# Kernel tuning notes

Measured on AMD Instinct MI355X. Metric: run time of the kernel, lower is better.

The kernel has to match this reference:

```python
import jax, jax.numpy as jnp
import numpy as np

N_NODES = 100000
N_EDGES = 1600000
IN_CH = 128
EDGE_CH = 16
OUT_CH = 64
H1, F1 = 8, 8          # gat1: heads=8, out=8, concat -> 64
NEG_SLOPE = 0.2


def _add_self_loops(edge_index, n):
    sl = jnp.arange(n, dtype=edge_index.dtype)
    return jnp.concatenate([edge_index, jnp.stack([sl, sl])], axis=1)


def gat_layer(x, edge_index, W, a_src, a_dst, b, heads, out_dim, concat):
    """PyG-style GATConv (eval mode, self-loops already included in edge_index)."""
    n = x.shape[0]
    src, dst = edge_index[0], edge_index[1]
    xW = (x @ W).reshape(n, heads, out_dim)          # [N,H,F]
    al_src = (xW * a_src).sum(-1)                    # [N,H]
    al_dst = (xW * a_dst).sum(-1)                    # [N,H]
    e = jax.nn.leaky_relu(al_src[src] + al_dst[dst], NEG_SLOPE)  # [E,H]
    # segment softmax over incoming edges of each dst node
    m = jnp.full((n, heads), -jnp.inf, e.dtype).at[dst].max(e)
    w = jnp.exp(e - m[dst])
    denom = jax.ops.segment_sum(w, dst, num_segments=n)
    alpha = w / (denom[dst] + 1e-16)                 # [E,H]
    out = jax.ops.segment_sum(xW[src] * alpha[..., None], dst, num_segments=n)
    out = out.reshape(n, heads * out_dim) if concat else out.mean(axis=1)
    return out + b


def setup_inputs() -> dict:
    key = jax.random.key(0)
    ks = jax.random.split(key, 16)
    p = lambda k, shp: (jax.random.normal(k, shp, jnp.float32) * 0.1)
    inp = {
        "x": jax.random.normal(ks[0], (N_NODES, IN_CH), jnp.float32),
        "edge_index": jax.random.randint(ks[1], (2, N_EDGES), 0, N_NODES, jnp.int64 if jax.config.jax_enable_x64 else jnp.int32),
        "edge_attr": jax.random.normal(ks[2], (N_EDGES, EDGE_CH), jnp.float32),
        "W1": p(ks[3], (IN_CH, H1 * F1)),
        "a_src1": p(ks[4], (H1, F1)),
        "a_dst1": p(ks[5], (H1, F1)),
        "b1": jnp.zeros((H1 * F1,), jnp.float32),
        "W2": p(ks[6], (H1 * F1, OUT_CH)),
        "a_src2": p(ks[7], (1, OUT_CH)),
        "a_dst2": p(ks[8], (1, OUT_CH)),
        "b2": jnp.zeros((OUT_CH,), jnp.float32),
        "lin_W": p(ks[9], (OUT_CH, OUT_CH)),
        "lin_b": jnp.zeros((OUT_CH,), jnp.float32),
        "mlp_W1": p(ks[10], (2 * OUT_CH + EDGE_CH, 128)),
        "mlp_b1": jnp.zeros((128,), jnp.float32),
        "mlp_W2": p(ks[11], (128, 2)),
        "mlp_b2": jnp.zeros((2,), jnp.float32),
    }
    return inp


def reference(x, edge_index, edge_attr, W1, a_src1, a_dst1, b1, W2, a_src2, a_dst2, b2,
              lin_W, lin_b, mlp_W1, mlp_b1, mlp_W2, mlp_b2):
    n = x.shape[0]
    ei_sl = _add_self_loops(edge_index, n)
    h = gat_layer(x, ei_sl, W1, a_src1, a_dst1, b1, H1, F1, concat=True)
    h = jax.nn.elu(h)
    h = gat_layer(h, ei_sl, W2, a_src2, a_dst2, b2, 1, OUT_CH, concat=False)
    h = jax.nn.elu(h)
    h = h @ lin_W + lin_b                              # [N, out]
    src, dst = edge_index[0], edge_index[1]
    ef = jnp.concatenate([h[src], h[dst], edge_attr], axis=1)  # [E, 2*out+edge_ch]
    eo = jax.nn.relu(ef @ mlp_W1 + mlp_b1) @ mlp_W2 + mlp_b2   # [E, 2]
    return jax.nn.log_softmax(eo, axis=1)
```

## Files before the change

kernel.cpp:

```cpp
#include <hip/hip_runtime.h>
#include <math.h>

#define DEV_INLINE __device__ __forceinline__
typedef unsigned short ushort;
typedef __attribute__((ext_vector_type(8))) short bf16x8;
typedef __attribute__((ext_vector_type(4))) float f32x4;

DEV_INLINE float lrelu(float x){ return x > 0.f ? x : 0.2f*x; }
DEV_INLINE float eluf(float x){ return x>0.f? x : (__expf(x)-1.f); }
DEV_INLINE ushort f2bf(float f){
  unsigned u = __float_as_uint(f);
  return (ushort)((u + 0x7FFFu + ((u>>16)&1u)) >> 16);
}

__global__ __launch_bounds__(256) void gemm_n64(const float* __restrict__ A, const float* __restrict__ W,
    const float* __restrict__ bias, float* __restrict__ C, ushort* __restrict__ Cb, int n, int K)
{
  int j = threadIdx.x & 63;
  int node = blockIdx.x*4 + (threadIdx.x>>6);
  if (node >= n) return;
  const float4* A4 = (const float4*)(A + (size_t)node*K);
  float acc = 0.f;
  int K4 = K>>2;
  for (int k4 = 0; k4 < K4; ++k4) {
    float4 a = A4[k4];
    const float* w = W + k4*256 + j;
    acc = fmaf(a.x, w[0],   acc);
    acc = fmaf(a.y, w[64],  acc);
    acc = fmaf(a.z, w[128], acc);
    acc = fmaf(a.w, w[192], acc);
  }
  if (bias) acc += bias[j];
  if (C)  C[(size_t)node*64 + j] = acc;
  if (Cb) Cb[(size_t)node*64 + j] = f2bf(acc);
}

__global__ __launch_bounds__(256) void hist_kernel(const int* __restrict__ dst, int* __restrict__ deg, int E)
{
  int e = blockIdx.x*blockDim.x + threadIdx.x;
  if (e < E) atomicAdd(deg + dst[e], 1);
}

__global__ __launch_bounds__(256) void scan_p1(const int* __restrict__ deg, int* __restrict__ part, int n)
{
  __shared__ int red[256];
  int base = blockIdx.x*1024;
  int s = 0;
  for (int k = threadIdx.x; k < 1024; k += 256) { int i = base+k; s += (i<n)? deg[i] : 0; }
  red[threadIdx.x] = s; __syncthreads();
  for (int off = 128; off > 0; off >>= 1) {
    if (threadIdx.x < off) red[threadIdx.x] += red[threadIdx.x+off];
    __syncthreads();
  }
  if (threadIdx.x == 0) part[blockIdx.x] = red[0];
}

__global__ void scan_p2(int* part, int* rowptr, int nb, int n)
{
  if (threadIdx.x == 0 && blockIdx.x == 0) {
    int run = 0;
    for (int b = 0; b < nb; ++b) { int v = part[b]; part[b] = run; run += v; }
    rowptr[n] = run;
  }
}

__global__ __launch_bounds__(256) void scan_p3(const int* __restrict__ deg, const int* __restrict__ part,
    int* __restrict__ rowptr, int n)
{
  __shared__ int ts[256];
  int tid = threadIdx.x;
  int base = blockIdx.x*1024 + tid*4;
  int v0=0,v1=0,v2=0,v3=0;
  if (base+0 < n) v0 = deg[base+0];
  if (base+1 < n) v1 = deg[base+1];
  if (base+2 < n) v2 = deg[base+2];
  if (base+3 < n) v3 = deg[base+3];
  ts[tid] = v0+v1+v2+v3; __syncthreads();
  for (int off = 1; off < 256; off <<= 1) {
    int t = (tid >= off) ? ts[tid-off] : 0;
    __syncthreads();
    ts[tid] += t;
    __syncthreads();
  }
  int ex = part[blockIdx.x] + (tid ? ts[tid-1] : 0);
  if (base+0 < n) { rowptr[base+0] = ex; ex += v0; }
  if (base+1 < n) { rowptr[base+1] = ex; ex += v1; }
  if (base+2 < n) { rowptr[base+2] = ex; ex += v2; }
  if (base+3 < n) { rowptr[base+3] = ex; ex += v3; }
}

__global__ __launch_bounds__(256) void copy_int(const int* __restrict__ a, int* __restrict__ b, int n)
{
  int i = blockIdx.x*blockDim.x + threadIdx.x;
  if (i < n) b[i] = a[i];
}

__global__ __launch_bounds__(256) void scatter_kernel(const int* __restrict__ src, const int* __restrict__ dst,
    int* __restrict__ cursor, int* __restrict__ csr, int E)
{
  int e = blockIdx.x*blockDim.x + threadIdx.x;
  if (e >= E) return;
  int pos = atomicAdd(cursor + dst[e], 1);
  csr[pos] = src[e];
}

__global__ __launch_bounds__(256) void al_init1(const float* __restrict__ xW, const float* __restrict__ a_src,
    const float* __restrict__ a_dst, float* __restrict__ alS, float* __restrict__ alD, int n)
{
  int t = blockIdx.x*blockDim.x + threadIdx.x;
  if (t >= n*8) return;
  int h = t & 7;
  const float4* xw4 = (const float4*)(xW + (size_t)(t>>3)*64 + h*8);
  float4 x0 = xw4[0], x1 = xw4[1];
  const float4* as4 = (const float4*)(a_src + h*8);
  const float4* ad4 = (const float4*)(a_dst + h*8);
  float4 s0 = as4[0], s1 = as4[1], d0 = ad4[0], d1 = ad4[1];
  alS[t] = x0.x*s0.x + x0.y*s0.y + x0.z*s0.z + x0.w*s0.w
         + x1.x*s1.x + x1.y*s1.y + x1.z*s1.z + x1.w*s1.w;
  alD[t] = x0.x*d0.x + x0.y*d0.y + x0.z*d0.z + x0.w*d0.w
         + x1.x*d1.x + x1.y*d1.y + x1.z*d1.z + x1.w*d1.w;
}

__global__ __launch_bounds__(256) void al_init2(const float* __restrict__ xW, const float* __restrict__ a_src,
    const float* __restrict__ a_dst, float* __restrict__ alS, float* __restrict__ alD, int n)
{
  int node = blockIdx.x*blockDim.x + threadIdx.x;
  if (node >= n) return;
  const float4* xw4 = (const float4*)(xW + (size_t)node*64);
  const float4* as4 = (const float4*)a_src;
  const float4* ad4 = (const float4*)a_dst;
  float s = 0.f, d = 0.f;
  #pragma unroll
  for (int q = 0; q < 16; ++q) {
    float4 v = xw4[q], a = as4[q], bb = ad4[q];
    s += v.x*a.x + v.y*a.y + v.z*a.z + v.w*a.w;
    d += v.x*bb.x + v.y*bb.y + v.z*bb.z + v.w*bb.w;
  }
  alS[node] = s; alD[node] = d;
}

__global__ __launch_bounds__(256) void agg1(const float* __restrict__ xW, const float* __restrict__ alS,
    const float* __restrict__ alD, const int* __restrict__ rowptr, const int* __restrict__ csr,
    const float* __restrict__ b, float* __restrict__ outp, int n)
{
  int node = blockIdx.x*4 + (threadIdx.x>>6);
  if (node >= n) return;
  int l = threadIdx.x & 63, h = l >> 3;
  float aD  = alD[(size_t)node*8 + h];
  float m   = lrelu(alS[(size_t)node*8 + h] + aD);
  float den = 1.f;
  float acc = xW[(size_t)node*64 + l];
  int p0 = rowptr[node], p1 = rowptr[node+1];
  for (int p = p0; p < p1; ++p) {
    int s = csr[p];
    float e  = lrelu(alS[(size_t)s*8 + h] + aD);
    float xv = xW[(size_t)s*64 + l];
    float mn = fmaxf(m, e);
    float sc = __expf(m - mn);
    float w  = __expf(e - mn);
    den = den*sc + w;
    acc = acc*sc + w*xv;
    m = mn;
  }
  outp[(size_t)node*64 + l] = eluf(acc/(den + 1e-16f) + b[l]);
}

__global__ __launch_bounds__(256) void agg2(const float* __restrict__ xW, const float* __restrict__ alS,
    const float* __restrict__ alD, const int* __restrict__ rowptr, const int* __restrict__ csr,
    const float* __restrict__ b, float* __restrict__ outp, int n)
{
  int node = blockIdx.x*4 + (threadIdx.x>>6);
  if (node >= n) return;
  int l = threadIdx.x & 63;
  float aD  = alD[node];
  float m   = lrelu(alS[node] + aD);
  float den = 1.f;
  float acc = xW[(size_t)node*64 + l];
  int p0 = rowptr[node], p1 = rowptr[node+1];
  for (int p = p0; p < p1; ++p) {
    int s = csr[p];
    float e  = lrelu(alS[s] + aD);
    float xv = xW[(size_t)s*64 + l];
    float mn = fmaxf(m, e);
    float sc = __expf(m - mn);
    float w  = __expf(e - mn);
    den = den*sc + w;
    acc = acc*sc + w*xv;
    m = mn;
  }
  outp[(size_t)node*64 + l] = eluf(acc/(den + 1e-16f) + b[l]);
}

__global__ __launch_bounds__(256) void attr2bf(const float* __restrict__ attr, ushort* __restrict__ attrb, int n4)
{
  int t = blockIdx.x*blockDim.x + threadIdx.x;
  if (t >= n4) return;
  float4 a = ((const float4*)attr)[t];
  ushort4 o; o.x = f2bf(a.x); o.y = f2bf(a.y); o.z = f2bf(a.z); o.w = f2bf(a.w);
  ((ushort4*)attrb)[t] = o;
}

__global__ void w1_swizzle(const float* __restrict__ W1, ushort* __restrict__ w1sw)
{
  int t = blockIdx.x*blockDim.x + threadIdx.x;
  if (t >= 2560) return;
  int l = t & 63, nk = t >> 6;
  int nt = nk/5, ks = nk - nt*5;
  int ncol = nt*16 + (l&15);
  int kb = ks*32 + (l>>4)*8;
  union { ushort u[8]; uint4 q; } v;
  #pragma unroll
  for (int j = 0; j < 8; ++j) {
    int k = kb + j;
    float f = (k < 144) ? W1[k*128 + ncol] : 0.f;
    v.u[j] = f2bf(f);
  }
  ((uint4*)w1sw)[t] = v.q;
}

__global__ __launch_bounds__(256) void edge_mlp_mfma(
    const ushort* __restrict__ h3b, const ushort* __restrict__ attrb,
    const int* __restrict__ src, const int* __restrict__ dst,
    const ushort* __restrict__ w1sw, const float* __restrict__ b1,
    const float* __restrict__ W2, const float* __restrict__ b2,
    float* __restrict__ out, int E)
{
  __shared__ uint4 W1s[2560];
  for (int i = threadIdx.x; i < 2560; i += 256) W1s[i] = ((const uint4*)w1sw)[i];
  __syncthreads();
  const bf16x8* Bf = (const bf16x8*)W1s;

  const int lane = threadIdx.x & 63;
  const int quad = lane >> 4, l15 = lane & 15;

  float w2a[8], w2b[8], bia[8];
  #pragma unroll
  for (int nt = 0; nt < 8; ++nt) {
    w2a[nt] = W2[(nt*16 + l15)*2 + 0];
    w2b[nt] = W2[(nt*16 + l15)*2 + 1];
    bia[nt] = b1[nt*16 + l15];
  }
  const float bb0 = b2[0], bb1 = b2[1];

  const int wid = (blockIdx.x*256 + threadIdx.x) >> 6;
  const int nw  = gridDim.x*4;
  const int nT  = (E + 15) >> 4;

  for (int t = wid; t < nT; t += nw) {
    const int tb = t*16;
    int e = tb + l15; if (e >= E) e = E - 1;
    const int s = src[e], d = dst[e];

    bf16x8 a0 = *(const bf16x8*)(h3b + (size_t)s*64 + quad*8);
    bf16x8 a1 = *(const bf16x8*)(h3b + (size_t)s*64 + 32 + quad*8);
    bf16x8 a2 = *(const bf16x8*)(h3b + (size_t)d*64 + quad*8);
    bf16x8 a3 = *(const bf16x8*)(h3b + (size_t)d*64 + 32 + quad*8);
    bf16x8 a4 = {};
    if (quad < 2) a4 = *(const bf16x8*)(attrb + (size_t)e*16 + quad*8);

    f32x4 acc[8];
    #pragma unroll
    for (int nt = 0; nt < 8; ++nt) acc[nt] = (f32x4){0.f,0.f,0.f,0.f};

    #pragma unroll
    for (int nt = 0; nt < 8; ++nt) {
      acc[nt] = __builtin_amdgcn_mfma_f32_16x16x32_bf16(a0, Bf[(nt*5+0)*64 + lane], acc[nt], 0,0,0);
      acc[nt] = __builtin_amdgcn_mfma_f32_16x16x32_bf16(a1, Bf[(nt*5+1)*64 + lane], acc[nt], 0,0,0);
      acc[nt] = __builtin_amdgcn_mfma_f32_16x16x32_bf16(a2, Bf[(nt*5+2)*64 + lane], acc[nt], 0,0,0);
      acc[nt] = __builtin_amdgcn_mfma_f32_16x16x32_bf16(a3, Bf[(nt*5+3)*64 + lane], acc[nt], 0,0,0);
      acc[nt] = __builtin_amdgcn_mfma_f32_16x16x32_bf16(a4, Bf[(nt*5+4)*64 + lane], acc[nt], 0,0,0);
    }

    #pragma unroll
    for (int r = 0; r < 4; ++r) {
      float p0 = 0.f, p1 = 0.f;
      #pragma unroll
      for (int nt = 0; nt < 8; ++nt) {
        float hv = fmaxf(acc[nt][r] + bia[nt], 0.f);
        p0 = fmaf(hv, w2a[nt], p0);
        p1 = fmaf(hv, w2b[nt], p1);
      }
      #pragma unroll
      for (int off = 1; off < 16; off <<= 1) {
        p0 += __shfl_xor(p0, off, 64);
        p1 += __shfl_xor(p1, off, 64);
      }
      if (l15 == 0) {
        int eo = tb + quad*4 + r;
        if (eo < E) {
          p0 += bb0; p1 += bb1;
          float mm = fmaxf(p0, p1);
          float ls = mm + __logf(__expf(p0-mm) + __expf(p1-mm));
          ((float2*)out)[eo] = make_float2(p0 - ls, p1 - ls);
        }
      }
    }
  }
}

extern "C" void kernel_launch(void* const* d_in, const int* in_sizes, int n_in,
                              void* d_out, int out_size, void* d_ws, size_t ws_size,
                              hipStream_t stream) {
  const float* x      = (const float*)d_in[0];
  const int*   ei     = (const int*)d_in[1];
  const float* attr   = (const float*)d_in[2];
  const float* W1     = (const float*)d_in[3];
  const float* a_src1 = (const float*)d_in[4];
  const float* a_dst1 = (const float*)d_in[5];
  const float* b1     = (const float*)d_in[6];
  const float* W2     = (const float*)d_in[7];
  const float* a_src2 = (const float*)d_in[8];
  const float* a_dst2 = (const float*)d_in[9];
  const float* b2     = (const float*)d_in[10];
  const float* linW   = (const float*)d_in[11];
  const float* linb   = (const float*)d_in[12];
  const float* mW1    = (const float*)d_in[13];
  const float* mb1    = (const float*)d_in[14];
  const float* mW2    = (const float*)d_in[15];
  const float* mb2    = (const float*)d_in[16];
  float* out = (float*)d_out;

  int N = in_sizes[0] / 128;
  int E = in_sizes[1] / 2;
  const int* src = ei;
  const int* dst = ei + E;

  char* ws = (char*)d_ws;
  float*    bufA   = (float*)(ws);
  float*    bufH   = (float*)(ws + 25600000);
  int*      csr    = (int*)  (ws + 51200000);
  float*    alS1   = (float*)(ws + 57600000);
  float*    alD1   = (float*)(ws + 60800000);
  int*      rowptr = (int*)  (ws + 64000000);
  int*      degcur = (int*)  (ws + 64400064);
  int*      part   = (int*)  (ws + 64800064);
  ushort*   w1sw   = (ushort*)(ws + 64900096);
  float*    alS2   = (float*)(ws + 57600000);
  float*    alD2   = (float*)(ws + 58000000);
  ushort*   h3b    = (ushort*)(ws + 51200000);
  ushort*   attrb  = (ushort*)(ws);

  int gN4 = (N + 3) / 4;
  int gNH = (N*8 + 255) / 256;
  int gN  = (N + 255) / 256;
  int gE  = (E + 255) / 256;
  int nChunk = (N + 1023) / 1024;

  hipMemsetAsync(degcur, 0, (size_t)N*sizeof(int), stream);
  hist_kernel<<<gE, 256, 0, stream>>>(dst, degcur, E);
  scan_p1<<<nChunk, 256, 0, stream>>>(degcur, part, N);
  scan_p2<<<1, 64, 0, stream>>>(part, rowptr, nChunk, N);
  scan_p3<<<nChunk, 256, 0, stream>>>(degcur, part, rowptr, N);
  copy_int<<<gN, 256, 0, stream>>>(rowptr, degcur, N);
  scatter_kernel<<<gE, 256, 0, stream>>>(src, dst, degcur, csr, E);
  w1_swizzle<<<10, 256, 0, stream>>>(mW1, w1sw);

  gemm_n64<<<gN4, 256, 0, stream>>>(x, W1, nullptr, bufA, nullptr, N, 128);
  al_init1<<<gNH, 256, 0, stream>>>(bufA, a_src1, a_dst1, alS1, alD1, N);
  agg1<<<gN4, 256, 0, stream>>>(bufA, alS1, alD1, rowptr, csr, b1, bufH, N);
  gemm_n64<<<gN4, 256, 0, stream>>>(bufH, W2, nullptr, bufA, nullptr, N, 64);
  al_init2<<<gN, 256, 0, stream>>>(bufA, a_src2, a_dst2, alS2, alD2, N);
  agg2<<<gN4, 256, 0, stream>>>(bufA, alS2, alD2, rowptr, csr, b2, bufH, N);
  gemm_n64<<<gN4, 256, 0, stream>>>(bufH, linW, linb, nullptr, h3b, N, 64);
  attr2bf<<<(E*4 + 255)/256, 256, 0, stream>>>(attr, attrb, E*4);
  edge_mlp_mfma<<<1024, 256, 0, stream>>>(h3b, attrb, src, dst, w1sw, mb1, mW2, mb2, out, E);
}
```

Baseline: 1.336 ms.

## Store GAT features in bf16, fuse attr conversion and cursor copy, unroll aggregation

The node-feature buffers xW for both GAT layers are now stored as bf16, halving gather traffic in the aggregation kernels and the attention-logit kernels. The separate copy_int and attr2bf kernels are removed: the scan writes the cursor directly, and edge_attr is converted to bf16 inside the edge MLP. The aggregation loops are unrolled by two, and the edge MLP gets more blocks and an occupancy hint. The bf16 storage lowers the precision of intermediate features.

```diff
diff --git a/kernel.cpp b/kernel.cpp
--- a/kernel.cpp
+++ b/kernel.cpp
@@ -12,9 +12,10 @@
   unsigned u = __float_as_uint(f);
   return (ushort)((u + 0x7FFFu + ((u>>16)&1u)) >> 16);
 }
+DEV_INLINE float b2f(ushort u){ return __uint_as_float(((unsigned)u)<<16); }
 
 __global__ __launch_bounds__(256) void gemm_n64(const float* __restrict__ A, const float* __restrict__ W,
-    const float* __restrict__ bias, float* __restrict__ C, ushort* __restrict__ Cb, int n, int K)
+    const float* __restrict__ bias, ushort* __restrict__ Cb, int n, int K)
 {
   int j = threadIdx.x & 63;
   int node = blockIdx.x*4 + (threadIdx.x>>6);
@@ -31,8 +32,7 @@
     acc = fmaf(a.w, w[192], acc);
   }
   if (bias) acc += bias[j];
-  if (C)  C[(size_t)node*64 + j] = acc;
-  if (Cb) Cb[(size_t)node*64 + j] = f2bf(acc);
+  Cb[(size_t)node*64 + j] = f2bf(acc);
 }
 
 __global__ __launch_bounds__(256) void hist_kernel(const int* __restrict__ dst, int* __restrict__ deg, int E)
@@ -65,7 +65,7 @@
 }
 
 __global__ __launch_bounds__(256) void scan_p3(const int* __restrict__ deg, const int* __restrict__ part,
-    int* __restrict__ rowptr, int n)
+    int* __restrict__ rowptr, int* __restrict__ cursor, int n)
 {
   __shared__ int ts[256];
   int tid = threadIdx.x;
@@ -83,16 +83,10 @@
     __syncthreads();
   }
   int ex = part[blockIdx.x] + (tid ? ts[tid-1] : 0);
-  if (base+0 < n) { rowptr[base+0] = ex; ex += v0; }
-  if (base+1 < n) { rowptr[base+1] = ex; ex += v1; }
-  if (base+2 < n) { rowptr[base+2] = ex; ex += v2; }
-  if (base+3 < n) { rowptr[base+3] = ex; ex += v3; }
-}
-
-__global__ __launch_bounds__(256) void copy_int(const int* __restrict__ a, int* __restrict__ b, int n)
-{
-  int i = blockIdx.x*blockDim.x + threadIdx.x;
-  if (i < n) b[i] = a[i];
+  if (base+0 < n) { rowptr[base+0] = ex; cursor[base+0] = ex; ex += v0; }
+  if (base+1 < n) { rowptr[base+1] = ex; cursor[base+1] = ex; ex += v1; }
+  if (base+2 < n) { rowptr[base+2] = ex; cursor[base+2] = ex; ex += v2; }
+  if (base+3 < n) { rowptr[base+3] = ex; cursor[base+3] = ex; ex += v3; }
 }
 
 __global__ __launch_bounds__(256) void scatter_kernel(const int* __restrict__ src, const int* __restrict__ dst,
@@ -104,42 +98,44 @@
   csr[pos] = src[e];
 }
 
-__global__ __launch_bounds__(256) void al_init1(const float* __restrict__ xW, const float* __restrict__ a_src,
+__global__ __launch_bounds__(256) void al_init1(const ushort* __restrict__ xWb, const float* __restrict__ a_src,
     const float* __restrict__ a_dst, float* __restrict__ alS, float* __restrict__ alD, int n)
 {
   int t = blockIdx.x*blockDim.x + threadIdx.x;
   if (t >= n*8) return;
   int h = t & 7;
-  const float4* xw4 = (const float4*)(xW + (size_t)(t>>3)*64 + h*8);
-  float4 x0 = xw4[0], x1 = xw4[1];
+  bf16x8 v = *(const bf16x8*)(xWb + (size_t)(t>>3)*64 + h*8);
   const float4* as4 = (const float4*)(a_src + h*8);
   const float4* ad4 = (const float4*)(a_dst + h*8);
   float4 s0 = as4[0], s1 = as4[1], d0 = ad4[0], d1 = ad4[1];
-  alS[t] = x0.x*s0.x + x0.y*s0.y + x0.z*s0.z + x0.w*s0.w
-         + x1.x*s1.x + x1.y*s1.y + x1.z*s1.z + x1.w*s1.w;
-  alD[t] = x0.x*d0.x + x0.y*d0.y + x0.z*d0.z + x0.w*d0.w
-         + x1.x*d1.x + x1.y*d1.y + x1.z*d1.z + x1.w*d1.w;
-}
-
-__global__ __launch_bounds__(256) void al_init2(const float* __restrict__ xW, const float* __restrict__ a_src,
+  float x0 = b2f((ushort)v[0]), x1 = b2f((ushort)v[1]), x2 = b2f((ushort)v[2]), x3 = b2f((ushort)v[3]);
+  float x4 = b2f((ushort)v[4]), x5 = b2f((ushort)v[5]), x6 = b2f((ushort)v[6]), x7 = b2f((ushort)v[7]);
+  alS[t] = x0*s0.x + x1*s0.y + x2*s0.z + x3*s0.w + x4*s1.x + x5*s1.y + x6*s1.z + x7*s1.w;
+  alD[t] = x0*d0.x + x1*d0.y + x2*d0.z + x3*d0.w + x4*d1.x + x5*d1.y + x6*d1.z + x7*d1.w;
+}
+
+__global__ __launch_bounds__(256) void al_init2(const ushort* __restrict__ xWb, const float* __restrict__ a_src,
     const float* __restrict__ a_dst, float* __restrict__ alS, float* __restrict__ alD, int n)
 {
   int node = blockIdx.x*blockDim.x + threadIdx.x;
   if (node >= n) return;
-  const float4* xw4 = (const float4*)(xW + (size_t)node*64);
-  const float4* as4 = (const float4*)a_src;
-  const float4* ad4 = (const float4*)a_dst;
+  const bf16x8* xw8 = (const bf16x8*)(xWb + (size_t)node*64);
   float s = 0.f, d = 0.f;
   #pragma unroll
-  for (int q = 0; q < 16; ++q) {
-    float4 v = xw4[q], a = as4[q], bb = ad4[q];
-    s += v.x*a.x + v.y*a.y + v.z*a.z + v.w*a.w;
-    d += v.x*bb.x + v.y*bb.y + v.z*bb.z + v.w*bb.w;
+  for (int q = 0; q < 8; ++q) {
+    bf16x8 v = xw8[q];
+    const float4* a4 = (const float4*)(a_src + q*8);
+    const float4* b4 = (const float4*)(a_dst + q*8);
+    float4 a0 = a4[0], a1 = a4[1], c0 = b4[0], c1 = b4[1];
+    s += b2f((ushort)v[0])*a0.x + b2f((ushort)v[1])*a0.y + b2f((ushort)v[2])*a0.z + b2f((ushort)v[3])*a0.w
+       + b2f((ushort)v[4])*a1.x + b2f((ushort)v[5])*a1.y + b2f((ushort)v[6])*a1.z + b2f((ushort)v[7])*a1.w;
+    d += b2f((ushort)v[0])*c0.x + b2f((ushort)v[1])*c0.y + b2f((ushort)v[2])*c0.z + b2f((ushort)v[3])*c0.w
+       + b2f((ushort)v[4])*c1.x + b2f((ushort)v[5])*c1.y + b2f((ushort)v[6])*c1.z + b2f((ushort)v[7])*c1.w;
   }
   alS[node] = s; alD[node] = d;
 }
 
-__global__ __launch_bounds__(256) void agg1(const float* __restrict__ xW, const float* __restrict__ alS,
+__global__ __launch_bounds__(256) void agg1(const ushort* __restrict__ xWb, const float* __restrict__ alS,
     const float* __restrict__ alD, const int* __restrict__ rowptr, const int* __restrict__ csr,
     const float* __restrict__ b, float* __restrict__ outp, int n)
 {
@@ -149,23 +145,37 @@
   float aD  = alD[(size_t)node*8 + h];
   float m   = lrelu(alS[(size_t)node*8 + h] + aD);
   float den = 1.f;
-  float acc = xW[(size_t)node*64 + l];
-  int p0 = rowptr[node], p1 = rowptr[node+1];
-  for (int p = p0; p < p1; ++p) {
-    int s = csr[p];
-    float e  = lrelu(alS[(size_t)s*8 + h] + aD);
-    float xv = xW[(size_t)s*64 + l];
-    float mn = fmaxf(m, e);
+  float acc = b2f(xWb[(size_t)node*64 + l]);
+  int p = rowptr[node], p1 = rowptr[node+1];
+  for (; p+1 < p1; p += 2) {
+    int s0 = csr[p], s1 = csr[p+1];
+    float e0 = lrelu(alS[(size_t)s0*8 + h] + aD);
+    float e1 = lrelu(alS[(size_t)s1*8 + h] + aD);
+    float x0 = b2f(xWb[(size_t)s0*64 + l]);
+    float x1 = b2f(xWb[(size_t)s1*64 + l]);
+    float mn = fmaxf(m, fmaxf(e0, e1));
     float sc = __expf(m - mn);
-    float w  = __expf(e - mn);
-    den = den*sc + w;
-    acc = acc*sc + w*xv;
+    float w0 = __expf(e0 - mn);
+    float w1 = __expf(e1 - mn);
+    den = den*sc + w0 + w1;
+    acc = acc*sc + w0*x0 + w1*x1;
     m = mn;
   }
+  if (p < p1) {
+    int s0 = csr[p];
+    float e0 = lrelu(alS[(size_t)s0*8 + h] + aD);
+    float x0 = b2f(xWb[(size_t)s0*64 + l]);
+    float mn = fmaxf(m, e0);
+    float sc = __expf(m - mn);
+    float w0 = __expf(e0 - mn);
+    den = den*sc + w0;
+    acc = acc*sc + w0*x0;
+    m = mn;
+  }
   outp[(size_t)node*64 + l] = eluf(acc/(den + 1e-16f) + b[l]);
 }
 
-__global__ __launch_bounds__(256) void agg2(const float* __restrict__ xW, const float* __restrict__ alS,
+__global__ __launch_bounds__(256) void agg2(const ushort* __restrict__ xWb, const float* __restrict__ alS,
     const float* __restrict__ alD, const int* __restrict__ rowptr, const int* __restrict__ csr,
     const float* __restrict__ b, float* __restrict__ outp, int n)
 {
@@ -175,29 +185,34 @@
   float aD  = alD[node];
   float m   = lrelu(alS[node] + aD);
   float den = 1.f;
-  float acc = xW[(size_t)node*64 + l];
-  int p0 = rowptr[node], p1 = rowptr[node+1];
-  for (int p = p0; p < p1; ++p) {
-    int s = csr[p];
-    float e  = lrelu(alS[s] + aD);
-    float xv = xW[(size_t)s*64 + l];
-    float mn = fmaxf(m, e);
+  float acc = b2f(xWb[(size_t)node*64 + l]);
+  int p = rowptr[node], p1 = rowptr[node+1];
+  for (; p+1 < p1; p += 2) {
+    int s0 = csr[p], s1 = csr[p+1];
+    float e0 = lrelu(alS[s0] + aD);
+    float e1 = lrelu(alS[s1] + aD);
+    float x0 = b2f(xWb[(size_t)s0*64 + l]);
+    float x1 = b2f(xWb[(size_t)s1*64 + l]);
+    float mn = fmaxf(m, fmaxf(e0, e1));
     float sc = __expf(m - mn);
-    float w  = __expf(e - mn);
-    den = den*sc + w;
-    acc = acc*sc + w*xv;
+    float w0 = __expf(e0 - mn);
+    float w1 = __expf(e1 - mn);
+    den = den*sc + w0 + w1;
+    acc = acc*sc + w0*x0 + w1*x1;
     m = mn;
   }
+  if (p < p1) {
+    int s0 = csr[p];
+    float e0 = lrelu(alS[s0] + aD);
+    float x0 = b2f(xWb[(size_t)s0*64 + l]);
+    float mn = fmaxf(m, e0);
+    float sc = __expf(m - mn);
+    float w0 = __expf(e0 - mn);
+    den = den*sc + w0;
+    acc = acc*sc + w0*x0;
+    m = mn;
+  }
   outp[(size_t)node*64 + l] = eluf(acc/(den + 1e-16f) + b[l]);
-}
-
-__global__ __launch_bounds__(256) void attr2bf(const float* __restrict__ attr, ushort* __restrict__ attrb, int n4)
-{
-  int t = blockIdx.x*blockDim.x + threadIdx.x;
-  if (t >= n4) return;
-  float4 a = ((const float4*)attr)[t];
-  ushort4 o; o.x = f2bf(a.x); o.y = f2bf(a.y); o.z = f2bf(a.z); o.w = f2bf(a.w);
-  ((ushort4*)attrb)[t] = o;
 }
 
 __global__ void w1_swizzle(const float* __restrict__ W1, ushort* __restrict__ w1sw)
@@ -218,8 +233,8 @@
   ((uint4*)w1sw)[t] = v.q;
 }
 
-__global__ __launch_bounds__(256) void edge_mlp_mfma(
-    const ushort* __restrict__ h3b, const ushort* __restrict__ attrb,
+__global__ __launch_bounds__(256, 4) void edge_mlp_mfma(
+    const ushort* __restrict__ h3b, const float* __restrict__ attr,
     const int* __restrict__ src, const int* __restrict__ dst,
     const ushort* __restrict__ w1sw, const float* __restrict__ b1,
     const float* __restrict__ W2, const float* __restrict__ b2,
@@ -256,7 +271,14 @@
     bf16x8 a2 = *(const bf16x8*)(h3b + (size_t)d*64 + quad*8);
     bf16x8 a3 = *(const bf16x8*)(h3b + (size_t)d*64 + 32 + quad*8);
     bf16x8 a4 = {};
-    if (quad < 2) a4 = *(const bf16x8*)(attrb + (size_t)e*16 + quad*8);
+    if (quad < 2) {
+      const float4* ap = (const float4*)(attr + (size_t)e*16 + quad*8);
+      float4 f0 = ap[0], f1 = ap[1];
+      a4[0] = (short)f2bf(f0.x); a4[1] = (short)f2bf(f0.y);
+      a4[2] = (short)f2bf(f0.z); a4[3] = (short)f2bf(f0.w);
+      a4[4] = (short)f2bf(f1.x); a4[5] = (short)f2bf(f1.y);
+      a4[6] = (short)f2bf(f1.z); a4[7] = (short)f2bf(f1.w);
+    }
 
     f32x4 acc[8];
     #pragma unroll
@@ -326,19 +348,16 @@
   const int* dst = ei + E;
 
   char* ws = (char*)d_ws;
-  float*    bufA   = (float*)(ws);
-  float*    bufH   = (float*)(ws + 25600000);
+  float*    bufH   = (float*)(ws);
+  ushort*   bufAb  = (ushort*)(ws + 25600000);
+  ushort*   h3b    = (ushort*)(ws + 38400000);
   int*      csr    = (int*)  (ws + 51200000);
-  float*    alS1   = (float*)(ws + 57600000);
-  float*    alD1   = (float*)(ws + 60800000);
+  float*    alS    = (float*)(ws + 57600000);
+  float*    alD    = (float*)(ws + 60800000);
   int*      rowptr = (int*)  (ws + 64000000);
   int*      degcur = (int*)  (ws + 64400064);
   int*      part   = (int*)  (ws + 64800064);
   ushort*   w1sw   = (ushort*)(ws + 64900096);
-  float*    alS2   = (float*)(ws + 57600000);
-  float*    alD2   = (float*)(ws + 58000000);
-  ushort*   h3b    = (ushort*)(ws + 51200000);
-  ushort*   attrb  = (ushort*)(ws);
 
   int gN4 = (N + 3) / 4;
   int gNH = (N*8 + 255) / 256;
@@ -350,18 +369,16 @@
   hist_kernel<<<gE, 256, 0, stream>>>(dst, degcur, E);
   scan_p1<<<nChunk, 256, 0, stream>>>(degcur, part, N);
   scan_p2<<<1, 64, 0, stream>>>(part, rowptr, nChunk, N);
-  scan_p3<<<nChunk, 256, 0, stream>>>(degcur, part, rowptr, N);
-  copy_int<<<gN, 256, 0, stream>>>(rowptr, degcur, N);
+  scan_p3<<<nChunk, 256, 0, stream>>>(degcur, part, rowptr, degcur, N);
   scatter_kernel<<<gE, 256, 0, stream>>>(src, dst, degcur, csr, E);
   w1_swizzle<<<10, 256, 0, stream>>>(mW1, w1sw);
 
-  gemm_n64<<<gN4, 256, 0, stream>>>(x, W1, nullptr, bufA, nullptr, N, 128);
-  al_init1<<<gNH, 256, 0, stream>>>(bufA, a_src1, a_dst1, alS1, alD1, N);
-  agg1<<<gN4, 256, 0, stream>>>(bufA, alS1, alD1, rowptr, csr, b1, bufH, N);
-  gemm_n64<<<gN4, 256, 0, stream>>>(bufH, W2, nullptr, bufA, nullptr, N, 64);
-  al_init2<<<gN, 256, 0, stream>>>(bufA, a_src2, a_dst2, alS2, alD2, N);
-  agg2<<<gN4, 256, 0, stream>>>(bufA, alS2, alD2, rowptr, csr, b2, bufH, N);
-  gemm_n64<<<gN4, 256, 0, stream>>>(bufH, linW, linb, nullptr, h3b, N, 64);
-  attr2bf<<<(E*4 + 255)/256, 256, 0, stream>>>(attr, attrb, E*4);
-  edge_mlp_mfma<<<1024, 256, 0, stream>>>(h3b, attrb, src, dst, w1sw, mb1, mW2, mb2, out, E);
-}
+  gemm_n64<<<gN4, 256, 0, stream>>>(x, W1, nullptr, bufAb, N, 128);
+  al_init1<<<gNH, 256, 0, stream>>>(bufAb, a_src1, a_dst1, alS, alD, N);
+  agg1<<<gN4, 256, 0, stream>>>(bufAb, alS, alD, rowptr, csr, b1, bufH, N);
+  gemm_n64<<<gN4, 256, 0, stream>>>(bufH, W2, nullptr, bufAb, N, 64);
+  al_init2<<<gN, 256, 0, stream>>>(bufAb, a_src2, a_dst2, alS, alD, N);
+  agg2<<<gN4, 256, 0, stream>>>(bufAb, alS, alD, rowptr, csr, b2, bufH, N);
+  gemm_n64<<<gN4, 256, 0, stream>>>(bufH, linW, linb, h3b, N, 64);
+  edge_mlp_mfma<<<2048, 256, 0, stream>>>(h3b, attr, src, dst, w1sw, mb1, mW2, mb2, out, E);
+}
```

Result: slower. 1.510 ms (+13.0%).
